# Kernel optimization log

Hardware: AMD Instinct MI355X
Metric: run time of the kernel (lower is better)

## Reference

```python
import jax, jax.numpy as jnp
import numpy as np

EPS = 1e-6

def _rmsnorm(x, scale):
    # RMSNorm over last axis (TPNorm pre-norm)
    var = jnp.mean(jnp.square(x), axis=-1, keepdims=True)
    return x * jax.lax.rsqrt(var + EPS) * scale


def setup_inputs() -> dict:
    key = jax.random.key(0)
    ks = jax.random.split(key, 6)
    B, S, D, H, Dh = 2, 2048, 1024, 16, 64
    x = jax.random.normal(ks[0], (B, S, D), dtype=jnp.float32)
    norm_scale = jnp.ones((D,), dtype=jnp.float32)
    # lecun_normal-like scaling: std = 1/sqrt(fan_in)
    wq = jax.random.normal(ks[1], (D, H, Dh), dtype=jnp.float32) / np.sqrt(D)
    wk = jax.random.normal(ks[2], (D, H, Dh), dtype=jnp.float32) / np.sqrt(D)
    wv = jax.random.normal(ks[3], (D, H, Dh), dtype=jnp.float32) / np.sqrt(D)
    w_out = jax.random.normal(ks[4], (H, Dh, D), dtype=jnp.float32) / np.sqrt(H * Dh)
    b_out = jnp.zeros((D,), dtype=jnp.float32)
    return {"x": x, "norm_scale": norm_scale, "wq": wq, "wk": wk, "wv": wv,
            "w_out": w_out, "b_out": b_out}


def reference(x, norm_scale, wq, wk, wv, w_out, b_out):
    dtype = x.dtype
    softmax_dtype = jnp.float32
    h = _rmsnorm(x, norm_scale)                                  # [B,S,D]
    q = jnp.einsum('bsd,dhe->bshe', h, wq)                       # [B,S,H,Dh]
    k = jnp.einsum('bsd,dhe->bshe', h, wk)
    v = jnp.einsum('bsd,dhe->bshe', h, wv)
    head_dim = q.shape[-1]
    scale = head_dim ** (-0.5)
    q = (q * scale).astype(softmax_dtype)
    kf = k.astype(softmax_dtype)
    weights = jnp.einsum('bqhd,bkhd->bhqk', q, kf)               # [B,H,S,S] fp32
    weights = jax.nn.softmax(weights, axis=-1).astype(dtype)
    new_vals = jnp.einsum('bhqk,bkhd->bqhd', weights, v).astype(dtype)
    out = jnp.einsum('bqhe,hed->bqd', new_vals, w_out) + b_out   # [B,S,D]
    return out
```

## Files before the change

kernel.cpp:

```cpp
#include <hip/hip_runtime.h>

typedef unsigned short u16;
typedef unsigned int   u32;
typedef __attribute__((ext_vector_type(8))) short bf16x8;
typedef __attribute__((ext_vector_type(4))) float f32x4;

#define SEQ 2048
#define DIM 1024
#define NH  16
#define DH  64
#define NROW 4096

static __device__ __forceinline__ u16 f2bf(float f){
  u32 u; __builtin_memcpy(&u, &f, 4);
  u32 r = (u + 0x7fffu + ((u >> 16) & 1u)) >> 16;
  return (u16)r;
}
static __device__ __forceinline__ u32 pack2bf(float a, float b){
  u32 ua, ub; __builtin_memcpy(&ua, &a, 4); __builtin_memcpy(&ub, &b, 4);
  return ((ua + 0x8000u) >> 16) | ((ub + 0x8000u) & 0xFFFF0000u);
}
static __device__ __forceinline__ u32 cvt_pk_bf16(float a, float b){
  u32 r;
  asm("v_cvt_pk_bf16_f32 %0, %1, %2" : "=v"(r) : "v"(a), "v"(b));
  return r;
}

#define GLD_LDS(gp, lp) \
  __builtin_amdgcn_global_load_lds( \
      (const __attribute__((address_space(1))) void*)(gp), \
      (__attribute__((address_space(3))) void*)(lp), 16, 0, 0)

#define WAIT_VM(N) asm volatile("s_waitcnt vmcnt(" #N ")" ::: "memory")
#define CFENCE()   asm volatile("" ::: "memory")

__global__ __launch_bounds__(256) void k_rmsnorm(const float* __restrict__ x,
                                                 const float* __restrict__ sc,
                                                 u16* __restrict__ h){
  int row = blockIdx.x, t = threadIdx.x;
  float4 v = ((const float4*)(x + (size_t)row * DIM))[t];
  float ss = v.x*v.x + v.y*v.y + v.z*v.z + v.w*v.w;
  #pragma unroll
  for (int d = 32; d; d >>= 1) ss += __shfl_down(ss, d, 64);
  __shared__ float red[4];
  if ((t & 63) == 0) red[t >> 6] = ss;
  __syncthreads();
  float tot = red[0] + red[1] + red[2] + red[3];
  float rms = rsqrtf(tot * (1.0f / DIM) + 1e-6f);
  float4 s4 = ((const float4*)sc)[t];
  u16 ov[4];
  ov[0] = f2bf(v.x * rms * s4.x);
  ov[1] = f2bf(v.y * rms * s4.y);
  ov[2] = f2bf(v.z * rms * s4.z);
  ov[3] = f2bf(v.w * rms * s4.w);
  ((uint2*)(h + (size_t)row * DIM))[t] = *(uint2*)ov;
}

__global__ __launch_bounds__(256) void k_wtrans(const float* __restrict__ in0,
                                                const float* __restrict__ in1,
                                                const float* __restrict__ in2,
                                                u16* __restrict__ outT){
  __shared__ u16 tile[64][68];
  int t = threadIdx.x;
  int c0 = blockIdx.x * 64;
  int r0 = blockIdx.y * 64;
  int z = blockIdx.z;
  const float* in = (z == 0) ? in0 : ((z == 1) ? in1 : in2);
  u16* out = outT + (size_t)z * (1u << 20);
  #pragma unroll
  for (int i = 0; i < 4; i++){
    int idx = t + 256 * i;
    int r = idx >> 4, c4 = (idx & 15) * 4;
    float4 v = *(const float4*)&in[(size_t)(r0 + r) * 1024 + c0 + c4];
    u16 pk[4] = {f2bf(v.x), f2bf(v.y), f2bf(v.z), f2bf(v.w)};
    *(uint2*)&tile[r][c4] = *(uint2*)pk;
  }
  __syncthreads();
  #pragma unroll
  for (int i = 0; i < 2; i++){
    int c = t + 256 * i;
    int n = c >> 3, koff = (c & 7) * 8;
    alignas(16) u16 vals[8];
    #pragma unroll
    for (int j = 0; j < 8; j++) vals[j] = tile[koff + j][n];
    *(uint4*)&out[(size_t)(c0 + n) * 1024 + r0 + koff] = *(uint4*)vals;
  }
}

__global__ __launch_bounds__(256) void k_gemm(const u16* __restrict__ A,
                                              const u16* __restrict__ B0,
                                              const u16* __restrict__ B1,
                                              const u16* __restrict__ B2,
                                              void* __restrict__ C0,
                                              void* __restrict__ C1,
                                              void* __restrict__ C2,
                                              const float* __restrict__ bias,
                                              int qkv){
  __shared__ u16 Al[3][128][32];
  __shared__ u16 Bl[3][128][32];
  int t = threadIdx.x, lane = t & 63, w = t >> 6;
  int wm = w & 1, wn = w >> 1;
  int mrow = lane & 15, quad = lane >> 4;

  int nwgs = qkv ? 768 : 256;
  int cpx = nwgs >> 3;
  int id = blockIdx.x;
  int wg = (id & 7) * cpx + (id >> 3);
  int z = wg >> 8;
  int rem = wg & 255;
  int m0 = (rem >> 3) << 7;
  int n0 = (rem & 7) << 7;
  const u16* Bt = (z == 0) ? B0 : ((z == 1) ? B1 : B2);

  int r0s = (t * 16) >> 6, off0 = ((t * 16) & 63) >> 1;
  int r1s = r0s + 64;

  const u16* Ap0 = &A [(size_t)(m0 + r0s) * 1024 + off0];
  const u16* Ap1 = &A [(size_t)(m0 + r1s) * 1024 + off0];
  const u16* Bp0 = &Bt[(size_t)(n0 + r0s) * 1024 + off0];
  const u16* Bp1 = &Bt[(size_t)(n0 + r1s) * 1024 + off0];

  f32x4 acc[4][4];
  #pragma unroll
  for (int ms = 0; ms < 4; ms++)
    #pragma unroll
    for (int ns = 0; ns < 4; ns++) acc[ms][ns] = (f32x4){0.f, 0.f, 0.f, 0.f};

  GLD_LDS(Ap0,      &Al[0][r0s][off0]);
  GLD_LDS(Ap1,      &Al[0][r1s][off0]);
  GLD_LDS(Bp0,      &Bl[0][r0s][off0]);
  GLD_LDS(Bp1,      &Bl[0][r1s][off0]);
  GLD_LDS(Ap0 + 32, &Al[1][r0s][off0]);
  GLD_LDS(Ap1 + 32, &Al[1][r1s][off0]);
  GLD_LDS(Bp0 + 32, &Bl[1][r0s][off0]);
  GLD_LDS(Bp1 + 32, &Bl[1][r1s][off0]);

  int cur = 0, pf = 2;
  for (int kt = 0; kt < 32; kt++){
    if (kt < 31) WAIT_VM(4); else WAIT_VM(0);
    __builtin_amdgcn_s_barrier();
    CFENCE();
    if (kt < 30){
      int K2 = (kt + 2) * 32;
      GLD_LDS(Ap0 + K2, &Al[pf][r0s][off0]);
      GLD_LDS(Ap1 + K2, &Al[pf][r1s][off0]);
      GLD_LDS(Bp0 + K2, &Bl[pf][r0s][off0]);
      GLD_LDS(Bp1 + K2, &Bl[pf][r1s][off0]);
    }
    bf16x8 af[4], bfr[4];
    #pragma unroll
    for (int ms = 0; ms < 4; ms++)
      af[ms] = *(const bf16x8*)&Al[cur][wm * 64 + ms * 16 + mrow][quad * 8];
    #pragma unroll
    for (int ns = 0; ns < 4; ns++)
      bfr[ns] = *(const bf16x8*)&Bl[cur][wn * 64 + ns * 16 + mrow][quad * 8];
    #pragma unroll
    for (int ms = 0; ms < 4; ms++)
      #pragma unroll
      for (int ns = 0; ns < 4; ns++)
        acc[ms][ns] = __builtin_amdgcn_mfma_f32_16x16x32_bf16(af[ms], bfr[ns], acc[ms][ns], 0, 0, 0);
    cur = (cur == 2) ? 0 : cur + 1;
    pf  = (pf  == 2) ? 0 : pf  + 1;
  }

  float qscale = (qkv && z == 0) ? 0.180336880111112f : 1.0f;
  bool  vmode  = (qkv && z == 2);
  void* C = (z == 0) ? C0 : ((z == 1) ? C1 : C2);

  #pragma unroll
  for (int ms = 0; ms < 4; ms++){
    #pragma unroll
    for (int ns = 0; ns < 4; ns++){
      int col = n0 + wn * 64 + ns * 16 + mrow;
      int rbase = m0 + wm * 64 + ms * 16 + quad * 4;
      if (vmode){
        int b = rbase >> 11, sl = rbase & 2047;
        int hh = col >> 6, e = col & 63;
        uint2 pk = { pack2bf(acc[ms][ns][0], acc[ms][ns][1]),
                     pack2bf(acc[ms][ns][2], acc[ms][ns][3]) };
        *(uint2*)&((u16*)C)[(size_t)((b * NH + hh) * DH + e) * SEQ + sl] = pk;
      } else if (qkv){
        #pragma unroll
        for (int r = 0; r < 4; r++)
          ((u16*)C)[(size_t)(rbase + r) * 1024 + col] = f2bf(acc[ms][ns][r] * qscale);
      } else {
        float bv = bias ? bias[col] : 0.f;
        #pragma unroll
        for (int r = 0; r < 4; r++)
          ((float*)C)[(size_t)(rbase + r) * 1024 + col] = acc[ms][ns][r] + bv;
      }
    }
  }
}

__global__ __launch_bounds__(512) void k_attn(const u16* q,
                                              const u16* __restrict__ k,
                                              const u16* __restrict__ vt,
                                              u16* nv){
  __shared__ u16 Kl[3][64][64];
  __shared__ u16 Vl[3][64][64];
  int t = threadIdx.x, lane = t & 63, w = t >> 6;
  int mrow = lane & 15, quad = lane >> 4;
  int id = blockIdx.x;
  int wg = (id & 7) * 64 + (id >> 3);
  int s0 = (wg & 15) * 128;
  int bh = wg >> 4; int b = bh >> 4, hh = bh & 15;

  const u16* qrow = q + (size_t)((b * SEQ + s0 + w * 16 + mrow) * NH + hh) * DH;
  bf16x8 bq0 = *(const bf16x8*)(qrow + quad * 8);
  bf16x8 bq1 = *(const bf16x8*)(qrow + 32 + quad * 8);

  int rw  = t >> 3;
  int fst = (rw & 3) | (((t >> 6) & 1) << 2);
  int lc  = (t & 7) ^ fst;
  const u16* kp = k  + ((size_t)b * SEQ + rw) * (NH * DH) + hh * DH + lc * 8;
  const u16* vp = vt + ((size_t)bh * DH + rw) * SEQ + lc * 8;

  int row0 = ((mrow >> 2) << 3) | (mrow & 3);
  int cK = (quad ^ ((mrow & 3) | (((mrow >> 2) & 1) << 2))) << 4;
  int cV = (quad ^ ((mrow & 3) | (((mrow >> 3) & 1) << 2))) << 4;

  f32x4 o[4];
  #pragma unroll
  for (int g = 0; g < 4; g++) o[g] = (f32x4){0.f, 0.f, 0.f, 0.f};
  f32x4 accl = (f32x4){0.f, 0.f, 0.f, 0.f};
  bf16x8 onesf;
  #pragma unroll
  for (int j = 0; j < 8; j++) onesf[j] = (short)0x3F80;

  GLD_LDS(kp, (u16*)Kl[0] + (t << 3));
  GLD_LDS(vp, (u16*)Vl[0] + (t << 3));
  kp += 64 * NH * DH; vp += 64;
  GLD_LDS(kp, (u16*)Kl[1] + (t << 3));
  GLD_LDS(vp, (u16*)Vl[1] + (t << 3));
  kp += 64 * NH * DH; vp += 64;

  int cur = 0, pf = 2;
  for (int kt = 0; kt < 32; kt++){
    if (kt < 31) WAIT_VM(2); else WAIT_VM(0);
    __builtin_amdgcn_s_barrier();
    CFENCE();
    if (kt < 30){
      GLD_LDS(kp, (u16*)Kl[pf] + (t << 3));
      GLD_LDS(vp, (u16*)Vl[pf] + (t << 3));
      kp += 64 * NH * DH; vp += 64;
    }

    const char* Kb = (const char*)Kl[cur];
    f32x4 sT[4];
    __builtin_amdgcn_s_setprio(1);
    #pragma unroll
    for (int g = 0; g < 4; g++){
      int rg = row0 + ((g & 1) << 2) + ((g >> 1) << 5);
      const char* rp = Kb + rg * 128;
      bf16x8 a0 = *(const bf16x8*)(rp + cK);
      bf16x8 a1 = *(const bf16x8*)(rp + (cK ^ 64));
      f32x4 zz = (f32x4){0.f, 0.f, 0.f, 0.f};
      zz = __builtin_amdgcn_mfma_f32_16x16x32_bf16(a0, bq0, zz, 0, 0, 0);
      zz = __builtin_amdgcn_mfma_f32_16x16x32_bf16(a1, bq1, zz, 0, 0, 0);
      sT[g] = zz;
    }
    __builtin_amdgcn_s_setprio(0);

    u32 wd[8];
    #pragma unroll
    for (int g = 0; g < 4; g++){
      float e0 = exp2f(sT[g][0]), e1 = exp2f(sT[g][1]);
      float e2 = exp2f(sT[g][2]), e3 = exp2f(sT[g][3]);
      wd[g * 2]     = cvt_pk_bf16(e0, e1);
      wd[g * 2 + 1] = cvt_pk_bf16(e2, e3);
    }
    union { u32 u[4]; bf16x8 v; } U0, U1;
    U0.u[0] = wd[0]; U0.u[1] = wd[1]; U0.u[2] = wd[2]; U0.u[3] = wd[3];
    U1.u[0] = wd[4]; U1.u[1] = wd[5]; U1.u[2] = wd[6]; U1.u[3] = wd[7];
    bf16x8 pb0 = U0.v, pb1 = U1.v;

    __builtin_amdgcn_s_setprio(1);
    accl = __builtin_amdgcn_mfma_f32_16x16x32_bf16(onesf, pb0, accl, 0, 0, 0);
    accl = __builtin_amdgcn_mfma_f32_16x16x32_bf16(onesf, pb1, accl, 0, 0, 0);

    const char* Vb = (const char*)Vl[cur];
    #pragma unroll
    for (int ge = 0; ge < 4; ge++){
      const char* rp = Vb + (ge * 16 + mrow) * 128;
      bf16x8 v0 = *(const bf16x8*)(rp + cV);
      bf16x8 v1 = *(const bf16x8*)(rp + (cV ^ 64));
      o[ge] = __builtin_amdgcn_mfma_f32_16x16x32_bf16(v0, pb0, o[ge], 0, 0, 0);
      o[ge] = __builtin_amdgcn_mfma_f32_16x16x32_bf16(v1, pb1, o[ge], 0, 0, 0);
    }
    __builtin_amdgcn_s_setprio(0);

    cur = (cur == 2) ? 0 : cur + 1;
    pf  = (pf  == 2) ? 0 : pf  + 1;
  }

  float rl = 1.0f / accl[0];
  u16* orow = nv + (size_t)((b * SEQ + s0 + w * 16 + mrow) * NH + hh) * DH;
  #pragma unroll
  for (int ge = 0; ge < 4; ge++){
    uint2 pk = { cvt_pk_bf16(o[ge][0] * rl, o[ge][1] * rl),
                 cvt_pk_bf16(o[ge][2] * rl, o[ge][3] * rl) };
    *(uint2*)&orow[ge * 16 + quad * 4] = pk;
  }
}

extern "C" void kernel_launch(void* const* d_in, const int* in_sizes, int n_in,
                              void* d_out, int out_size, void* d_ws, size_t ws_size,
                              hipStream_t stream){
  const float* x   = (const float*)d_in[0];
  const float* nsc = (const float*)d_in[1];
  const float* wq  = (const float*)d_in[2];
  const float* wk  = (const float*)d_in[3];
  const float* wv  = (const float*)d_in[4];
  const float* wo  = (const float*)d_in[5];
  const float* bo  = (const float*)d_in[6];
  char* ws = (char*)d_ws;
  const size_t MB = (size_t)1 << 20;

  u16* qb  = (u16*)(ws);
  u16* kb  = (u16*)(ws + 8  * MB);
  u16* vtb = (u16*)(ws + 16 * MB);
  u16* h   = (u16*)d_out;
  u16* wT  = (u16*)((char*)d_out + 8 * MB);
  u16* wqT = wT;
  u16* wkT = wT + (1u << 20);
  u16* wvT = wT + (2u << 20);
  u16* woT = kb;

  k_rmsnorm<<<NROW, 256, 0, stream>>>(x, nsc, h);
  k_wtrans<<<dim3(16, 16, 3), 256, 0, stream>>>(wq, wk, wv, wT);
  k_gemm<<<dim3(768), 256, 0, stream>>>(h, wqT, wkT, wvT, qb, kb, vtb, nullptr, 1);
  k_attn<<<dim3(512), 512, 0, stream>>>(qb, kb, vtb, qb);
  k_wtrans<<<dim3(16, 16, 1), 256, 0, stream>>>(wo, wo, wo, woT);
  k_gemm<<<dim3(256), 256, 0, stream>>>(qb, woT, woT, woT, d_out, d_out, d_out, bo, 0);
}
```

Before: 210.6 us.

## Halve attention block threads, give each wave two 16-row query tiles

The attention kernel now runs with 256 threads (4 waves) per block instead of 512, and each wave handles 32 query rows as two 16-row groups. This reuses every K/V fragment read from LDS across two query tiles, cutting LDS reads per MFMA. Each thread now issues two K and two V global-to-LDS loads per tile, with the wait count adjusted to match. The exp2f calls also switch to the raw hardware builtin. The cost is higher register pressure and fewer waves per block to hide latency.

```diff
diff --git a/kernel.cpp b/kernel.cpp
--- a/kernel.cpp
+++ b/kernel.cpp
@@ -193,7 +193,7 @@
   }
 }
 
-__global__ __launch_bounds__(512) void k_attn(const u16* q,
+__global__ __launch_bounds__(256) void k_attn(const u16* q,
                                               const u16* __restrict__ k,
                                               const u16* __restrict__ vt,
                                               u16* nv){
@@ -206,9 +206,13 @@
   int s0 = (wg & 15) * 128;
   int bh = wg >> 4; int b = bh >> 4, hh = bh & 15;
 
-  const u16* qrow = q + (size_t)((b * SEQ + s0 + w * 16 + mrow) * NH + hh) * DH;
-  bf16x8 bq0 = *(const bf16x8*)(qrow + quad * 8);
-  bf16x8 bq1 = *(const bf16x8*)(qrow + 32 + quad * 8);
+  const u16* qrow0 = q + (size_t)((b * SEQ + s0 + w * 32 + mrow) * NH + hh) * DH;
+  const u16* qrow1 = qrow0 + 16 * NH * DH;
+  bf16x8 bq[2][2];
+  bq[0][0] = *(const bf16x8*)(qrow0 + quad * 8);
+  bq[0][1] = *(const bf16x8*)(qrow0 + 32 + quad * 8);
+  bq[1][0] = *(const bf16x8*)(qrow1 + quad * 8);
+  bq[1][1] = *(const bf16x8*)(qrow1 + 32 + quad * 8);
 
   int rw  = t >> 3;
   int fst = (rw & 3) | (((t >> 6) & 1) << 2);
@@ -220,34 +224,44 @@
   int cK = (quad ^ ((mrow & 3) | (((mrow >> 2) & 1) << 2))) << 4;
   int cV = (quad ^ ((mrow & 3) | (((mrow >> 3) & 1) << 2))) << 4;
 
-  f32x4 o[4];
-  #pragma unroll
-  for (int g = 0; g < 4; g++) o[g] = (f32x4){0.f, 0.f, 0.f, 0.f};
-  f32x4 accl = (f32x4){0.f, 0.f, 0.f, 0.f};
+  f32x4 o[2][4];
+  #pragma unroll
+  for (int qg = 0; qg < 2; qg++)
+    #pragma unroll
+    for (int g = 0; g < 4; g++) o[qg][g] = (f32x4){0.f, 0.f, 0.f, 0.f};
+  f32x4 accl[2];
+  accl[0] = (f32x4){0.f, 0.f, 0.f, 0.f};
+  accl[1] = (f32x4){0.f, 0.f, 0.f, 0.f};
   bf16x8 onesf;
   #pragma unroll
   for (int j = 0; j < 8; j++) onesf[j] = (short)0x3F80;
 
-  GLD_LDS(kp, (u16*)Kl[0] + (t << 3));
-  GLD_LDS(vp, (u16*)Vl[0] + (t << 3));
-  kp += 64 * NH * DH; vp += 64;
-  GLD_LDS(kp, (u16*)Kl[1] + (t << 3));
-  GLD_LDS(vp, (u16*)Vl[1] + (t << 3));
-  kp += 64 * NH * DH; vp += 64;
+  #pragma unroll
+  for (int pt = 0; pt < 2; pt++){
+    u16* dK = (u16*)Kl[pt]; u16* dV = (u16*)Vl[pt];
+    GLD_LDS(kp,                dK + (t << 3));
+    GLD_LDS(kp + 32 * NH * DH, dK + 2048 + (t << 3));
+    GLD_LDS(vp,                dV + (t << 3));
+    GLD_LDS(vp + 32 * SEQ,     dV + 2048 + (t << 3));
+    kp += 64 * NH * DH; vp += 64;
+  }
 
   int cur = 0, pf = 2;
   for (int kt = 0; kt < 32; kt++){
-    if (kt < 31) WAIT_VM(2); else WAIT_VM(0);
+    if (kt < 31) WAIT_VM(4); else WAIT_VM(0);
     __builtin_amdgcn_s_barrier();
     CFENCE();
     if (kt < 30){
-      GLD_LDS(kp, (u16*)Kl[pf] + (t << 3));
-      GLD_LDS(vp, (u16*)Vl[pf] + (t << 3));
+      u16* dK = (u16*)Kl[pf]; u16* dV = (u16*)Vl[pf];
+      GLD_LDS(kp,                dK + (t << 3));
+      GLD_LDS(kp + 32 * NH * DH, dK + 2048 + (t << 3));
+      GLD_LDS(vp,                dV + (t << 3));
+      GLD_LDS(vp + 32 * SEQ,     dV + 2048 + (t << 3));
       kp += 64 * NH * DH; vp += 64;
     }
 
     const char* Kb = (const char*)Kl[cur];
-    f32x4 sT[4];
+    f32x4 sT[2][4];
     __builtin_amdgcn_s_setprio(1);
     #pragma unroll
     for (int g = 0; g < 4; g++){
@@ -255,29 +269,41 @@
       const char* rp = Kb + rg * 128;
       bf16x8 a0 = *(const bf16x8*)(rp + cK);
       bf16x8 a1 = *(const bf16x8*)(rp + (cK ^ 64));
-      f32x4 zz = (f32x4){0.f, 0.f, 0.f, 0.f};
-      zz = __builtin_amdgcn_mfma_f32_16x16x32_bf16(a0, bq0, zz, 0, 0, 0);
-      zz = __builtin_amdgcn_mfma_f32_16x16x32_bf16(a1, bq1, zz, 0, 0, 0);
-      sT[g] = zz;
+      f32x4 z0 = (f32x4){0.f, 0.f, 0.f, 0.f};
+      f32x4 z1 = (f32x4){0.f, 0.f, 0.f, 0.f};
+      z0 = __builtin_amdgcn_mfma_f32_16x16x32_bf16(a0, bq[0][0], z0, 0, 0, 0);
+      z1 = __builtin_amdgcn_mfma_f32_16x16x32_bf16(a0, bq[1][0], z1, 0, 0, 0);
+      z0 = __builtin_amdgcn_mfma_f32_16x16x32_bf16(a1, bq[0][1], z0, 0, 0, 0);
+      z1 = __builtin_amdgcn_mfma_f32_16x16x32_bf16(a1, bq[1][1], z1, 0, 0, 0);
+      sT[0][g] = z0; sT[1][g] = z1;
     }
     __builtin_amdgcn_s_setprio(0);
 
-    u32 wd[8];
-    #pragma unroll
-    for (int g = 0; g < 4; g++){
-      float e0 = exp2f(sT[g][0]), e1 = exp2f(sT[g][1]);
-      float e2 = exp2f(sT[g][2]), e3 = exp2f(sT[g][3]);
-      wd[g * 2]     = cvt_pk_bf16(e0, e1);
-      wd[g * 2 + 1] = cvt_pk_bf16(e2, e3);
-    }
-    union { u32 u[4]; bf16x8 v; } U0, U1;
-    U0.u[0] = wd[0]; U0.u[1] = wd[1]; U0.u[2] = wd[2]; U0.u[3] = wd[3];
-    U1.u[0] = wd[4]; U1.u[1] = wd[5]; U1.u[2] = wd[6]; U1.u[3] = wd[7];
-    bf16x8 pb0 = U0.v, pb1 = U1.v;
+    bf16x8 pb[2][2];
+    #pragma unroll
+    for (int qg = 0; qg < 2; qg++){
+      u32 wd[8];
+      #pragma unroll
+      for (int g = 0; g < 4; g++){
+        float e0 = __builtin_amdgcn_exp2f(sT[qg][g][0]);
+        float e1 = __builtin_amdgcn_exp2f(sT[qg][g][1]);
+        float e2 = __builtin_amdgcn_exp2f(sT[qg][g][2]);
+        float e3 = __builtin_amdgcn_exp2f(sT[qg][g][3]);
+        wd[g * 2]     = cvt_pk_bf16(e0, e1);
+        wd[g * 2 + 1] = cvt_pk_bf16(e2, e3);
+      }
+      union { u32 u[4]; bf16x8 v; } U0, U1;
+      U0.u[0] = wd[0]; U0.u[1] = wd[1]; U0.u[2] = wd[2]; U0.u[3] = wd[3];
+      U1.u[0] = wd[4]; U1.u[1] = wd[5]; U1.u[2] = wd[6]; U1.u[3] = wd[7];
+      pb[qg][0] = U0.v; pb[qg][1] = U1.v;
+    }
 
     __builtin_amdgcn_s_setprio(1);
-    accl = __builtin_amdgcn_mfma_f32_16x16x32_bf16(onesf, pb0, accl, 0, 0, 0);
-    accl = __builtin_amdgcn_mfma_f32_16x16x32_bf16(onesf, pb1, accl, 0, 0, 0);
+    #pragma unroll
+    for (int qg = 0; qg < 2; qg++){
+      accl[qg] = __builtin_amdgcn_mfma_f32_16x16x32_bf16(onesf, pb[qg][0], accl[qg], 0, 0, 0);
+      accl[qg] = __builtin_amdgcn_mfma_f32_16x16x32_bf16(onesf, pb[qg][1], accl[qg], 0, 0, 0);
+    }
 
     const char* Vb = (const char*)Vl[cur];
     #pragma unroll
@@ -285,8 +311,10 @@
       const char* rp = Vb + (ge * 16 + mrow) * 128;
       bf16x8 v0 = *(const bf16x8*)(rp + cV);
       bf16x8 v1 = *(const bf16x8*)(rp + (cV ^ 64));
-      o[ge] = __builtin_amdgcn_mfma_f32_16x16x32_bf16(v0, pb0, o[ge], 0, 0, 0);
-      o[ge] = __builtin_amdgcn_mfma_f32_16x16x32_bf16(v1, pb1, o[ge], 0, 0, 0);
+      o[0][ge] = __builtin_amdgcn_mfma_f32_16x16x32_bf16(v0, pb[0][0], o[0][ge], 0, 0, 0);
+      o[1][ge] = __builtin_amdgcn_mfma_f32_16x16x32_bf16(v0, pb[1][0], o[1][ge], 0, 0, 0);
+      o[0][ge] = __builtin_amdgcn_mfma_f32_16x16x32_bf16(v1, pb[0][1], o[0][ge], 0, 0, 0);
+      o[1][ge] = __builtin_amdgcn_mfma_f32_16x16x32_bf16(v1, pb[1][1], o[1][ge], 0, 0, 0);
     }
     __builtin_amdgcn_s_setprio(0);
 
@@ -294,13 +322,18 @@
     pf  = (pf  == 2) ? 0 : pf  + 1;
   }
 
-  float rl = 1.0f / accl[0];
-  u16* orow = nv + (size_t)((b * SEQ + s0 + w * 16 + mrow) * NH + hh) * DH;
+  float rl0 = 1.0f / accl[0][0];
+  float rl1 = 1.0f / accl[1][0];
+  u16* orow0 = nv + (size_t)((b * SEQ + s0 + w * 32 + mrow) * NH + hh) * DH;
+  u16* orow1 = orow0 + 16 * NH * DH;
   #pragma unroll
   for (int ge = 0; ge < 4; ge++){
-    uint2 pk = { cvt_pk_bf16(o[ge][0] * rl, o[ge][1] * rl),
-                 cvt_pk_bf16(o[ge][2] * rl, o[ge][3] * rl) };
-    *(uint2*)&orow[ge * 16 + quad * 4] = pk;
+    uint2 pk0 = { cvt_pk_bf16(o[0][ge][0] * rl0, o[0][ge][1] * rl0),
+                  cvt_pk_bf16(o[0][ge][2] * rl0, o[0][ge][3] * rl0) };
+    *(uint2*)&orow0[ge * 16 + quad * 4] = pk0;
+    uint2 pk1 = { cvt_pk_bf16(o[1][ge][0] * rl1, o[1][ge][1] * rl1),
+                  cvt_pk_bf16(o[1][ge][2] * rl1, o[1][ge][3] * rl1) };
+    *(uint2*)&orow1[ge * 16 + quad * 4] = pk1;
   }
 }
 
@@ -330,7 +363,7 @@
   k_rmsnorm<<<NROW, 256, 0, stream>>>(x, nsc, h);
   k_wtrans<<<dim3(16, 16, 3), 256, 0, stream>>>(wq, wk, wv, wT);
   k_gemm<<<dim3(768), 256, 0, stream>>>(h, wqT, wkT, wvT, qb, kb, vtb, nullptr, 1);
-  k_attn<<<dim3(512), 512, 0, stream>>>(qb, kb, vtb, qb);
+  k_attn<<<dim3(512), 256, 0, stream>>>(qb, kb, vtb, qb);
   k_wtrans<<<dim3(16, 16, 1), 256, 0, stream>>>(wo, wo, wo, woT);
   k_gemm<<<dim3(256), 256, 0, stream>>>(qb, woT, woT, woT, d_out, d_out, d_out, bo, 0);
 }
```

Measured after the change: 206.8 us. No clear change (-1.8%).
